# Optimization experiments

Measured on AMD Instinct MI355X. Metric: run time of the kernel, lower is better.

## Reference

```python
import jax, jax.numpy as jnp
import numpy as np
from jax import lax

B, R, C, K = 4, 512, 80, 100          # images, rois/img, fg classes, post_nms_top_k
NMS_TH, SCORE_TH = 0.3, 0.1
MEAN = jnp.zeros(4, jnp.float32)       # delta_mean
STD = jnp.ones(4, jnp.float32)         # delta_std
NEG = jnp.float32(-1e9)
DWH_CLIP = jnp.float32(4.135166556742356)  # log(1000/16), standard bbox_xform clip


def setup_inputs() -> dict:
    key = jax.random.key(0)
    k1, k2, k3, k4 = jax.random.split(key, 4)
    x1y1 = jax.random.uniform(k1, (B, R, 2), minval=0.0, maxval=800.0)
    wh = jax.random.uniform(k2, (B, R, 2), minval=16.0, maxval=220.0)
    batch_rois = jnp.concatenate([x1y1, jnp.minimum(x1y1 + wh, 1023.0)], axis=-1)
    bbox_score = jax.random.uniform(k3, (B * R, C + 1, 1, 1), dtype=jnp.float32)
    bbox_deltas = jax.random.normal(k4, (B * R, (C + 1) * 4, 1, 1), dtype=jnp.float32) * 0.2
    im_hw = jnp.full((B, 1, 1, 2), 1024, dtype=jnp.int32)
    return {"batch_rois": batch_rois, "bbox_score": bbox_score,
            "bbox_deltas": bbox_deltas, "im_hw": im_hw}


def _pairwise_iou(b):
    # b: [R, 4] (x1,y1,x2,y2) -> [R, R]
    area = (b[:, 2] - b[:, 0]) * (b[:, 3] - b[:, 1])
    lt = jnp.maximum(b[:, None, :2], b[None, :, :2])
    rb = jnp.minimum(b[:, None, 2:], b[None, :, 2:])
    wh = jnp.maximum(rb - lt, 0.0)
    inter = wh[..., 0] * wh[..., 1]
    return inter / (area[:, None] + area[None, :] - inter + 1e-9)


def _nms_one_class(boxes, scores):
    # boxes: [R,4], scores: [R] -> keep mask + score-sorted boxes/scores
    order = jnp.argsort(-scores)
    b = boxes[order]
    s = scores[order]
    iou = _pairwise_iou(b)  # [R, R]

    def body(sup, i):
        keep_i = jnp.logical_and(jnp.logical_not(sup[i]), s[i] > SCORE_TH)
        new = jnp.where(keep_i, jnp.logical_or(sup, iou[i] > NMS_TH), sup)
        new = new.at[i].set(sup[i])  # never self-suppress
        return new, keep_i

    _, keep = lax.scan(body, jnp.zeros(b.shape[0], bool), jnp.arange(b.shape[0]))
    return keep, b, s


def _decode(rois, deltas, hw):
    # rois: [R,4], deltas: [R,C,4], hw: [2] (h, w) -> decoded boxes [R,C,4]
    d = deltas * STD + MEAN
    w = rois[:, 2] - rois[:, 0]
    h = rois[:, 3] - rois[:, 1]
    cx = rois[:, 0] + 0.5 * w
    cy = rois[:, 1] + 0.5 * h
    dx, dy = d[..., 0], d[..., 1]
    dw = jnp.minimum(d[..., 2], DWH_CLIP)
    dh = jnp.minimum(d[..., 3], DWH_CLIP)
    pcx = dx * w[:, None] + cx[:, None]
    pcy = dy * h[:, None] + cy[:, None]
    pw = w[:, None] * jnp.exp(dw)
    ph = h[:, None] * jnp.exp(dh)
    x1 = jnp.clip(pcx - 0.5 * pw, 0.0, hw[1] - 1.0)
    y1 = jnp.clip(pcy - 0.5 * ph, 0.0, hw[0] - 1.0)
    x2 = jnp.clip(pcx + 0.5 * pw, 0.0, hw[1] - 1.0)
    y2 = jnp.clip(pcy + 0.5 * ph, 0.0, hw[0] - 1.0)
    return jnp.stack([x1, y1, x2, y2], axis=-1)


def reference(batch_rois, bbox_score, bbox_deltas, im_hw):
    scores = bbox_score.reshape(B, R, C + 1)[..., 1:]               # [B,R,C] (skip bg)
    deltas = bbox_deltas.reshape(B, R, C + 1, 4)[:, :, 1:, :]       # [B,R,C,4]
    hw = im_hw.reshape(B, 2).astype(jnp.float32)

    def per_image(rois, sc, dl, hw_i):
        boxes = _decode(rois, dl, hw_i)                              # [R,C,4]
        keep, bs, ss = jax.vmap(_nms_one_class)(
            jnp.swapaxes(boxes, 0, 1), sc.T)                         # [C,R]...
        cls = jnp.broadcast_to(jnp.arange(C, dtype=jnp.float32)[:, None], (C, R))
        flat_s = jnp.where(keep, ss, NEG).reshape(-1)                # [C*R]
        top_s, idx = lax.top_k(flat_s, K)
        tb = bs.reshape(-1, 4)[idx]
        tc = cls.reshape(-1)[idx]
        valid = top_s > NEG * 0.5
        row = jnp.concatenate([tb, top_s[:, None], tc[:, None]], axis=-1)  # [K,6]
        pad = jnp.concatenate([jnp.zeros((K, 5), jnp.float32),
                               -jnp.ones((K, 1), jnp.float32)], axis=-1)
        return jnp.where(valid[:, None], row, pad)

    return jax.vmap(per_image)(batch_rois, scores, deltas, hw)      # [B,K,6]
```

## Files before the change

kernel.cpp:

```cpp
#include <hip/hip_runtime.h>
#include <cstdint>

#define BB 4
#define RR 512
#define CC 80
#define KK 100
#define NMS_TH 0.3f
#define SCORE_TH 0.1f
#define DWH_CLIP 4.135166556742356f

typedef unsigned short u16;
typedef unsigned int u32;
typedef unsigned long long u64;

__device__ __forceinline__ u32 f32_sortable(float f) {
  u32 u = __float_as_uint(f);
  u32 mask = (u32)((int)u >> 31) | 0x80000000u;
  return u ^ mask;
}
__device__ __forceinline__ float sortable_to_f32(u32 s) {
  u32 u = (s & 0x80000000u) ? (s ^ 0x80000000u) : ~s;
  return __uint_as_float(u);
}

__global__ __launch_bounds__(512) void nms_fused(
    const float* __restrict__ rois,
    const float* __restrict__ scores,
    const float* __restrict__ deltas,
    const int*   __restrict__ im_hw,
    u64*   __restrict__ cand_key,
    float4* __restrict__ cand_box)
{
#pragma clang fp contract(off)
  const int bc = blockIdx.x;
  const int b = bc / CC, c = bc % CC;
  const int tid = threadIdx.x;
  const int lane = tid & 63, wv = tid >> 6;

  __shared__ u64    keyarr[RR];
  __shared__ float4 box_s[RR];
  __shared__ float  sco_s[RR];
  __shared__ u64    rmk[64];
  __shared__ u64    supacc;
  __shared__ float4 kbox[KK];
  __shared__ float  ksc[KK];
  __shared__ float  karea[KK];
  __shared__ int    nkept_s;

  const float fh = (float)im_hw[b * 2 + 0] - 1.0f;
  const float fw = (float)im_hw[b * 2 + 1] - 1.0f;

  {
    const float sc = scores[(b * RR + tid) * (CC + 1) + (c + 1)];
    u64 v = ((u64)(~f32_sortable(sc)) << 32) | (u32)tid;
    const u32 t = (u32)tid;
    for (u32 kk = 2; kk <= RR; kk <<= 1) {
      for (u32 j = kk >> 1; j > 0; j >>= 1) {
        u64 p;
        if (j >= 64) {
          keyarr[t] = v;
          __syncthreads();
          p = keyarr[t ^ j];
          __syncthreads();
        } else {
          p = __shfl_xor(v, (int)j);
        }
        bool up = ((t & kk) == 0);
        bool lower = ((t & j) == 0);
        bool takemin = (up == lower);
        bool pless = (p < v);
        v = (takemin == pless) ? p : v;
      }
    }
    keyarr[t] = v;
  }
  __syncthreads();

  {
    const u64 kv = keyarr[tid];
    const int r = (int)(kv & 0xFFFFFFFFull);
    const float sc = sortable_to_f32(~(u32)(kv >> 32));
    const float4 roi = *(const float4*)&rois[(b * RR + r) * 4];
    const int base = (b * RR + r) * (CC + 1) + (c + 1);
    const float4 d = *(const float4*)&deltas[base * 4];

    float w  = roi.z - roi.x;
    float h  = roi.w - roi.y;
    float cx = roi.x + 0.5f * w;
    float cy = roi.y + 0.5f * h;
    float dw = fminf(d.z, DWH_CLIP);
    float dh = fminf(d.w, DWH_CLIP);
    float pcx = d.x * w + cx;
    float pcy = d.y * h + cy;
    float pw = w * expf(dw);
    float ph = h * expf(dh);
    float hx = 0.5f * pw, hy = 0.5f * ph;
    float x1 = fminf(fmaxf(pcx - hx, 0.0f), fw);
    float y1 = fminf(fmaxf(pcy - hy, 0.0f), fh);
    float x2 = fminf(fmaxf(pcx + hx, 0.0f), fw);
    float y2 = fminf(fmaxf(pcy + hy, 0.0f), fh);

    box_s[tid] = make_float4(x1, y1, x2, y2);
    sco_s[tid] = sc;
    if (tid == 0) nkept_s = 0;
  }
  __syncthreads();

  int nk = 0;
  for (int w = 0; w < 8; ++w) {
    const float4 bx = box_s[w * 64 + lane];
    const float  sc = sco_s[w * 64 + lane];
    const float  ar = (bx.z - bx.x) * (bx.w - bx.y);
    const float  areps = ar + 1e-9f;

    if (tid < 64) rmk[tid] = 0ull;
    if (tid == 64) supacc = 0ull;
    __syncthreads();

    {
      u64 myrow = 0;
      #pragma unroll
      for (int jj = 0; jj < 8; ++jj) {
        const int j = wv * 8 + jj;
        const float4 cb = box_s[w * 64 + j];
        const float ca = (cb.z - cb.x) * (cb.w - cb.y);
        float iw = fminf(bx.z, cb.z) - fmaxf(bx.x, cb.x);
        float ih = fminf(bx.w, cb.w) - fmaxf(bx.y, cb.y);
        iw = fmaxf(iw, 0.0f);
        ih = fmaxf(ih, 0.0f);
        const float inter = iw * ih;
        const float S = ca + areps;
        bool yes = inter * 4.3333247f > S;
        const bool no = inter * 4.3333420f < S;
        if (__any(!(yes || no))) {
          const float denom = ((ca + ar) - inter) + 1e-9f;
          const bool pe = inter / denom > NMS_TH;
          yes = (yes || no) ? yes : pe;
        }
        myrow |= yes ? (1ull << j) : 0ull;
      }
      myrow &= ~((2ull << lane) - 1ull);
      if (myrow) atomicOr(&rmk[lane], myrow);
    }

    {
      bool sup = false;
      for (int k = wv; k < nk; k += 8) {
        const float4 kb = kbox[k];
        const float  ka = karea[k];
        float iw = fminf(bx.z, kb.z) - fmaxf(bx.x, kb.x);
        float ih = fminf(bx.w, kb.w) - fmaxf(bx.y, kb.y);
        iw = fmaxf(iw, 0.0f);
        ih = fmaxf(ih, 0.0f);
        const float inter = iw * ih;
        const float S = ka + areps;
        bool yes = inter * 4.3333247f > S;
        const bool no = inter * 4.3333420f < S;
        if (__any(!(yes || no))) {
          const float denom = ((ka + ar) - inter) + 1e-9f;
          const bool pe = inter / denom > NMS_TH;
          yes = (yes || no) ? yes : pe;
        }
        sup = sup || yes;
      }
      const u64 bal = __ballot(sup);
      if (lane == 0 && bal) atomicOr(&supacc, bal);
    }
    __syncthreads();

    if (wv == 0) {
      u64 todo = __ballot(sc > SCORE_TH) & ~supacc;
      int nkl = nk;
      while (todo) {
        const int i = __ffsll((long long)todo) - 1;
        if (lane == 0) {
          const float4 kb = box_s[w * 64 + i];
          kbox[nkl] = kb;
          ksc[nkl] = sco_s[w * 64 + i];
          karea[nkl] = (kb.z - kb.x) * (kb.w - kb.y);
        }
        ++nkl;
        if (nkl >= KK) break;
        const u64 ri = rmk[i];
        todo &= ~((2ull << i) - 1ull);
        todo &= ~ri;
      }
      if (lane == 0) nkept_s = nkl;
    }
    __syncthreads();
    nk = nkept_s;
    if (nk >= KK) break;
  }

  if (tid < KK) {
    const int k = tid;
    u64 kv; float4 obx;
    if (k < nk) {
      kv = ((u64)(~f32_sortable(ksc[k])) << 32) | ((u64)(u32)c << 16) | (u32)k;
      obx = kbox[k];
    } else {
      kv = ((u64)(~f32_sortable(-1e9f)) << 32) | ((u64)(u32)c << 16) | (u32)k;
      obx = make_float4(0.f, 0.f, 0.f, 0.f);
    }
    cand_key[bc * KK + k] = kv;
    cand_box[bc * KK + k] = obx;
  }
}

__device__ __forceinline__ void sort128(u64* smallkeys, int tid) {
  u64 v = (tid < 128) ? smallkeys[tid] : ~0ull;
  const u32 t = (u32)tid;
  for (u32 kk = 2; kk <= 128; kk <<= 1) {
    for (u32 j = kk >> 1; j > 0; j >>= 1) {
      if (j >= 64) {
        if (tid < 128) smallkeys[t] = v;
        __syncthreads();
        u64 p = (tid < 128) ? smallkeys[t ^ j] : ~0ull;
        __syncthreads();
        if (tid < 128) {
          bool up = ((t & kk) == 0);
          bool lower = ((t & j) == 0);
          bool takemin = (up == lower);
          bool pless = (p < v);
          v = (takemin == pless) ? p : v;
        }
      } else if (tid < 128) {
        u64 p = __shfl_xor(v, (int)j);
        bool up = ((t & kk) == 0);
        bool lower = ((t & j) == 0);
        bool takemin = (up == lower);
        bool pless = (p < v);
        v = (takemin == pless) ? p : v;
      }
    }
  }
  if (tid < 128) smallkeys[t] = v;
  __syncthreads();
}

__global__ __launch_bounds__(1024) void topk_select(
    const u64* __restrict__ cand_key,
    const float4* __restrict__ cand_box,
    float* __restrict__ out)
{
  const int b = blockIdx.x;
  const int tid = threadIdx.x;
  const int lane = tid & 63, wv = tid >> 6;
  const int N = CC * KK;
  const u64* __restrict__ keys_g = cand_key + (size_t)b * N;

  __shared__ u16 candA[CC * KK];
  __shared__ u16 candB[CC * KK];
  __shared__ u32 whist[16][256];
  __shared__ u32 bins[256];
  __shared__ u64 smallkeys[128];
  __shared__ int ncand_s, rank_s, q_s;
  __shared__ u32 cnt_s;

  if (tid == 0) { ncand_s = N; rank_s = KK - 1; }

  u16* cur = candA;
  u16* oth = candB;
  bool first = true;
  int d = 7;
  for (;;) {
    for (int t = tid; t < 16 * 256; t += 1024) ((u32*)whist)[t] = 0;
    __syncthreads();
    const int nc = first ? N : ncand_s;
    const int sh = d * 8;
    for (int t0 = 0; t0 < nc; t0 += 1024) {
      const int t = t0 + tid;
      if (t < nc) {
        const int idx = first ? t : (int)cur[t];
        u32 dig = (u32)((keys_g[idx] >> sh) & 0xFF);
        atomicAdd(&whist[wv][dig], 1u);
      }
    }
    __syncthreads();
    if (tid < 256) {
      u32 s = 0;
      #pragma unroll
      for (int w = 0; w < 16; ++w) s += whist[w][tid];
      bins[tid] = s;
    }
    __syncthreads();
    if (wv == 0) {
      u32 c0 = bins[lane * 4 + 0], c1 = bins[lane * 4 + 1];
      u32 c2 = bins[lane * 4 + 2], c3 = bins[lane * 4 + 3];
      u32 lsum = c0 + c1 + c2 + c3;
      u32 incl = lsum;
      #pragma unroll
      for (int off = 1; off < 64; off <<= 1) {
        u32 v = __shfl_up(incl, off);
        if (lane >= off) incl += v;
      }
      u32 excl = incl - lsum;
      int rk = rank_s;
      u32 s0 = excl, s1 = excl + c0, s2 = s1 + c1, s3 = s2 + c2;
      int q = -1; u32 nr = 0;
      if (rk >= (int)s0 && rk < (int)(s0 + c0)) { q = lane * 4 + 0; nr = rk - s0; }
      else if (rk >= (int)s1 && rk < (int)(s1 + c1)) { q = lane * 4 + 1; nr = rk - s1; }
      else if (rk >= (int)s2 && rk < (int)(s2 + c2)) { q = lane * 4 + 2; nr = rk - s2; }
      else if (rk >= (int)s3 && rk < (int)(s3 + c3)) { q = lane * 4 + 3; nr = rk - s3; }
      if (q >= 0) { q_s = q; rank_s = (int)nr; }
    }
    if (tid == 0) cnt_s = 0;
    __syncthreads();
    const int q = q_s;
    for (int t0 = 0; t0 < nc; t0 += 1024) {
      const int t = t0 + tid;
      int idx = 0; bool m = false;
      if (t < nc) {
        idx = first ? t : (int)cur[t];
        m = ((int)((keys_g[idx] >> sh) & 0xFF) == q);
      }
      u64 bal = __ballot(m);
      u32 base = 0;
      if (lane == 0 && bal) base = atomicAdd(&cnt_s, (u32)__popcll(bal));
      base = __shfl(base, 0);
      if (m) oth[base + (u32)__popcll(bal & ((1ull << lane) - 1ull))] = (u16)idx;
    }
    __syncthreads();
    if (tid == 0) ncand_s = (int)cnt_s;
    { u16* tmp = cur; cur = oth; oth = tmp; }
    first = false;
    __syncthreads();
    if (ncand_s <= 128 || d == 0) break;
    --d;
  }

  u64 T;
  const int nc2 = ncand_s;
  if (nc2 == 1) {
    T = keys_g[cur[0]];
  } else {
    if (tid < 128) smallkeys[tid] = (tid < nc2) ? keys_g[cur[tid]] : ~0ull;
    __syncthreads();
    sort128(smallkeys, tid);
    T = smallkeys[rank_s];
    __syncthreads();
  }

  if (tid == 0) cnt_s = 0;
  if (tid < 128) smallkeys[tid] = ~0ull;
  __syncthreads();
  for (int t0 = 0; t0 < N; t0 += 1024) {
    const int t = t0 + tid;
    u64 k = 0; bool m = false;
    if (t < N) { k = keys_g[t]; m = (k <= T); }
    u64 bal = __ballot(m);
    u32 base = 0;
    if (lane == 0 && bal) base = atomicAdd(&cnt_s, (u32)__popcll(bal));
    base = __shfl(base, 0);
    if (m) {
      u32 p = base + (u32)__popcll(bal & ((1ull << lane) - 1ull));
      if (p < 128) smallkeys[p] = k;
    }
  }
  __syncthreads();

  sort128(smallkeys, tid);

  if (tid < KK) {
    const u64 kv = smallkeys[tid];
    const float s = sortable_to_f32(~(u32)(kv >> 32));
    float x1 = 0.f, y1 = 0.f, x2 = 0.f, y2 = 0.f, so = 0.f, cf = -1.0f;
    if (s > -5.0e8f) {
      int c = (int)((kv >> 16) & 0xFFFFull);
      int k = (int)(kv & 0xFFFFull);
      float4 bx = cand_box[((size_t)b * CC + c) * KK + k];
      x1 = bx.x; y1 = bx.y; x2 = bx.z; y2 = bx.w;
      so = s; cf = (float)c;
    }
    float* o = out + ((size_t)b * KK + tid) * 6;
    o[0] = x1; o[1] = y1; o[2] = x2; o[3] = y2; o[4] = so; o[5] = cf;
  }
}

extern "C" void kernel_launch(void* const* d_in, const int* in_sizes, int n_in,
                              void* d_out, int out_size, void* d_ws, size_t ws_size,
                              hipStream_t stream) {
  (void)in_sizes; (void)n_in; (void)out_size; (void)ws_size;
  const float* rois   = (const float*)d_in[0];
  const float* scores = (const float*)d_in[1];
  const float* deltas = (const float*)d_in[2];
  const int*   im_hw  = (const int*)d_in[3];

  char* ws = (char*)d_ws;
  u64*    cand_key = (u64*)ws;
  float4* cand_box = (float4*)(ws + 256000);

  nms_fused<<<BB * CC, 512, 0, stream>>>(rois, scores, deltas, im_hw,
                                         cand_key, cand_box);
  topk_select<<<BB, 1024, 0, stream>>>(cand_key, cand_box, (float*)d_out);
}
```

Baseline: 63.28 us.

## Fuse NMS and top-k into one kernel with last-block-done reduction

Merges the per-class NMS kernel and the per-image top-k selection kernel into a single launch. A global atomic counter per image lets the last finishing block run the radix-select top-k. The 512-element bitonic sort now keeps 8 keys per thread in registers, so fewer shared-memory round trips and barriers are needed. The intra-window suppression masks are precomputed for all 8 windows up front, and the greedy loop reads them with readlane instead of from shared memory. Top-k now runs with 512 threads instead of 1024 and needs a memset launch and threadfences, which may offset the saved kernel launch.

```diff
diff --git a/kernel.cpp b/kernel.cpp
--- a/kernel.cpp
+++ b/kernel.cpp
@@ -21,190 +21,6 @@
 __device__ __forceinline__ float sortable_to_f32(u32 s) {
   u32 u = (s & 0x80000000u) ? (s ^ 0x80000000u) : ~s;
   return __uint_as_float(u);
-}
-
-__global__ __launch_bounds__(512) void nms_fused(
-    const float* __restrict__ rois,
-    const float* __restrict__ scores,
-    const float* __restrict__ deltas,
-    const int*   __restrict__ im_hw,
-    u64*   __restrict__ cand_key,
-    float4* __restrict__ cand_box)
-{
-#pragma clang fp contract(off)
-  const int bc = blockIdx.x;
-  const int b = bc / CC, c = bc % CC;
-  const int tid = threadIdx.x;
-  const int lane = tid & 63, wv = tid >> 6;
-
-  __shared__ u64    keyarr[RR];
-  __shared__ float4 box_s[RR];
-  __shared__ float  sco_s[RR];
-  __shared__ u64    rmk[64];
-  __shared__ u64    supacc;
-  __shared__ float4 kbox[KK];
-  __shared__ float  ksc[KK];
-  __shared__ float  karea[KK];
-  __shared__ int    nkept_s;
-
-  const float fh = (float)im_hw[b * 2 + 0] - 1.0f;
-  const float fw = (float)im_hw[b * 2 + 1] - 1.0f;
-
-  {
-    const float sc = scores[(b * RR + tid) * (CC + 1) + (c + 1)];
-    u64 v = ((u64)(~f32_sortable(sc)) << 32) | (u32)tid;
-    const u32 t = (u32)tid;
-    for (u32 kk = 2; kk <= RR; kk <<= 1) {
-      for (u32 j = kk >> 1; j > 0; j >>= 1) {
-        u64 p;
-        if (j >= 64) {
-          keyarr[t] = v;
-          __syncthreads();
-          p = keyarr[t ^ j];
-          __syncthreads();
-        } else {
-          p = __shfl_xor(v, (int)j);
-        }
-        bool up = ((t & kk) == 0);
-        bool lower = ((t & j) == 0);
-        bool takemin = (up == lower);
-        bool pless = (p < v);
-        v = (takemin == pless) ? p : v;
-      }
-    }
-    keyarr[t] = v;
-  }
-  __syncthreads();
-
-  {
-    const u64 kv = keyarr[tid];
-    const int r = (int)(kv & 0xFFFFFFFFull);
-    const float sc = sortable_to_f32(~(u32)(kv >> 32));
-    const float4 roi = *(const float4*)&rois[(b * RR + r) * 4];
-    const int base = (b * RR + r) * (CC + 1) + (c + 1);
-    const float4 d = *(const float4*)&deltas[base * 4];
-
-    float w  = roi.z - roi.x;
-    float h  = roi.w - roi.y;
-    float cx = roi.x + 0.5f * w;
-    float cy = roi.y + 0.5f * h;
-    float dw = fminf(d.z, DWH_CLIP);
-    float dh = fminf(d.w, DWH_CLIP);
-    float pcx = d.x * w + cx;
-    float pcy = d.y * h + cy;
-    float pw = w * expf(dw);
-    float ph = h * expf(dh);
-    float hx = 0.5f * pw, hy = 0.5f * ph;
-    float x1 = fminf(fmaxf(pcx - hx, 0.0f), fw);
-    float y1 = fminf(fmaxf(pcy - hy, 0.0f), fh);
-    float x2 = fminf(fmaxf(pcx + hx, 0.0f), fw);
-    float y2 = fminf(fmaxf(pcy + hy, 0.0f), fh);
-
-    box_s[tid] = make_float4(x1, y1, x2, y2);
-    sco_s[tid] = sc;
-    if (tid == 0) nkept_s = 0;
-  }
-  __syncthreads();
-
-  int nk = 0;
-  for (int w = 0; w < 8; ++w) {
-    const float4 bx = box_s[w * 64 + lane];
-    const float  sc = sco_s[w * 64 + lane];
-    const float  ar = (bx.z - bx.x) * (bx.w - bx.y);
-    const float  areps = ar + 1e-9f;
-
-    if (tid < 64) rmk[tid] = 0ull;
-    if (tid == 64) supacc = 0ull;
-    __syncthreads();
-
-    {
-      u64 myrow = 0;
-      #pragma unroll
-      for (int jj = 0; jj < 8; ++jj) {
-        const int j = wv * 8 + jj;
-        const float4 cb = box_s[w * 64 + j];
-        const float ca = (cb.z - cb.x) * (cb.w - cb.y);
-        float iw = fminf(bx.z, cb.z) - fmaxf(bx.x, cb.x);
-        float ih = fminf(bx.w, cb.w) - fmaxf(bx.y, cb.y);
-        iw = fmaxf(iw, 0.0f);
-        ih = fmaxf(ih, 0.0f);
-        const float inter = iw * ih;
-        const float S = ca + areps;
-        bool yes = inter * 4.3333247f > S;
-        const bool no = inter * 4.3333420f < S;
-        if (__any(!(yes || no))) {
-          const float denom = ((ca + ar) - inter) + 1e-9f;
-          const bool pe = inter / denom > NMS_TH;
-          yes = (yes || no) ? yes : pe;
-        }
-        myrow |= yes ? (1ull << j) : 0ull;
-      }
-      myrow &= ~((2ull << lane) - 1ull);
-      if (myrow) atomicOr(&rmk[lane], myrow);
-    }
-
-    {
-      bool sup = false;
-      for (int k = wv; k < nk; k += 8) {
-        const float4 kb = kbox[k];
-        const float  ka = karea[k];
-        float iw = fminf(bx.z, kb.z) - fmaxf(bx.x, kb.x);
-        float ih = fminf(bx.w, kb.w) - fmaxf(bx.y, kb.y);
-        iw = fmaxf(iw, 0.0f);
-        ih = fmaxf(ih, 0.0f);
-        const float inter = iw * ih;
-        const float S = ka + areps;
-        bool yes = inter * 4.3333247f > S;
-        const bool no = inter * 4.3333420f < S;
-        if (__any(!(yes || no))) {
-          const float denom = ((ka + ar) - inter) + 1e-9f;
-          const bool pe = inter / denom > NMS_TH;
-          yes = (yes || no) ? yes : pe;
-        }
-        sup = sup || yes;
-      }
-      const u64 bal = __ballot(sup);
-      if (lane == 0 && bal) atomicOr(&supacc, bal);
-    }
-    __syncthreads();
-
-    if (wv == 0) {
-      u64 todo = __ballot(sc > SCORE_TH) & ~supacc;
-      int nkl = nk;
-      while (todo) {
-        const int i = __ffsll((long long)todo) - 1;
-        if (lane == 0) {
-          const float4 kb = box_s[w * 64 + i];
-          kbox[nkl] = kb;
-          ksc[nkl] = sco_s[w * 64 + i];
-          karea[nkl] = (kb.z - kb.x) * (kb.w - kb.y);
-        }
-        ++nkl;
-        if (nkl >= KK) break;
-        const u64 ri = rmk[i];
-        todo &= ~((2ull << i) - 1ull);
-        todo &= ~ri;
-      }
-      if (lane == 0) nkept_s = nkl;
-    }
-    __syncthreads();
-    nk = nkept_s;
-    if (nk >= KK) break;
-  }
-
-  if (tid < KK) {
-    const int k = tid;
-    u64 kv; float4 obx;
-    if (k < nk) {
-      kv = ((u64)(~f32_sortable(ksc[k])) << 32) | ((u64)(u32)c << 16) | (u32)k;
-      obx = kbox[k];
-    } else {
-      kv = ((u64)(~f32_sortable(-1e9f)) << 32) | ((u64)(u32)c << 16) | (u32)k;
-      obx = make_float4(0.f, 0.f, 0.f, 0.f);
-    }
-    cand_key[bc * KK + k] = kv;
-    cand_box[bc * KK + k] = obx;
-  }
 }
 
 __device__ __forceinline__ void sort128(u64* smallkeys, int tid) {
@@ -238,22 +54,226 @@
   __syncthreads();
 }
 
-__global__ __launch_bounds__(1024) void topk_select(
-    const u64* __restrict__ cand_key,
-    const float4* __restrict__ cand_box,
+__global__ __launch_bounds__(512) void nms_topk(
+    const float* __restrict__ rois,
+    const float* __restrict__ scores,
+    const float* __restrict__ deltas,
+    const int*   __restrict__ im_hw,
+    u32*   __restrict__ done_cnt,
+    u64*   __restrict__ cand_key,
+    float4* __restrict__ cand_box,
     float* __restrict__ out)
 {
-  const int b = blockIdx.x;
+#pragma clang fp contract(off)
+  const int bc = blockIdx.x;
+  const int b = bc / CC, c = bc % CC;
   const int tid = threadIdx.x;
   const int lane = tid & 63, wv = tid >> 6;
+
+  __shared__ __align__(16) char pool[42240];
+  float4* box_s = (float4*)pool;
+  float*  sco_s = (float*)(pool + 8192);
+  u64*    rmk_w = (u64*)(pool + 10240);
+  float4* kbox  = (float4*)(pool + 14336);
+  float*  ksc   = (float*)(pool + 15936);
+  float*  karea = (float*)(pool + 16336);
+  __shared__ u64 supacc_arr[8];
+  __shared__ int nkept_s, lastflag;
+
+  const float fh = (float)im_hw[b * 2 + 0] - 1.0f;
+  const float fw = (float)im_hw[b * 2 + 1] - 1.0f;
+
+  sco_s[tid] = scores[(b * RR + tid) * (CC + 1) + (c + 1)];
+  __syncthreads();
+
+  u64 k[8];
+  #pragma unroll
+  for (int r = 0; r < 8; ++r) {
+    const int e = r * 64 + lane;
+    k[r] = ((u64)(~f32_sortable(sco_s[e])) << 32) | (u32)e;
+  }
+  #pragma unroll
+  for (u32 kk2 = 2; kk2 <= 512; kk2 <<= 1) {
+    #pragma unroll
+    for (u32 j = 256; j > 0; j >>= 1) {
+      if (j > (kk2 >> 1)) continue;
+      if (j >= 64) {
+        const int dj = (int)(j >> 6);
+        #pragma unroll
+        for (int r = 0; r < 8; ++r) {
+          if ((r & dj) == 0) {
+            const int r2 = r | dj;
+            const bool up = (((u32)(r * 64) & kk2) == 0);
+            u64 a = k[r], b2 = k[r2];
+            const bool sw = up ? (a > b2) : (a < b2);
+            if (sw) { k[r] = b2; k[r2] = a; }
+          }
+        }
+      } else {
+        #pragma unroll
+        for (int r = 0; r < 8; ++r) {
+          u64 p = __shfl_xor(k[r], (int)j);
+          const u32 e = (u32)(r * 64) + (u32)lane;
+          const bool up = ((e & kk2) == 0);
+          const bool lower = (((u32)lane & j) == 0);
+          const bool takemin = (up == lower);
+          const bool pless = (p < k[r]);
+          k[r] = (takemin == pless) ? p : k[r];
+        }
+      }
+    }
+  }
+  __syncthreads();
+
+  {
+    u64 kv = k[0];
+    #pragma unroll
+    for (int r = 1; r < 8; ++r) if (wv == r) kv = k[r];
+    const int rr = (int)(kv & 0xFFFFFFFFull);
+    const float sc = sortable_to_f32(~(u32)(kv >> 32));
+    const float4 roi = *(const float4*)&rois[(b * RR + rr) * 4];
+    const int base = (b * RR + rr) * (CC + 1) + (c + 1);
+    const float4 d = *(const float4*)&deltas[base * 4];
+
+    float w  = roi.z - roi.x;
+    float h  = roi.w - roi.y;
+    float cx = roi.x + 0.5f * w;
+    float cy = roi.y + 0.5f * h;
+    float dw = fminf(d.z, DWH_CLIP);
+    float dh = fminf(d.w, DWH_CLIP);
+    float pcx = d.x * w + cx;
+    float pcy = d.y * h + cy;
+    float pw = w * expf(dw);
+    float ph = h * expf(dh);
+    float hx = 0.5f * pw, hy = 0.5f * ph;
+    float x1 = fminf(fmaxf(pcx - hx, 0.0f), fw);
+    float y1 = fminf(fmaxf(pcy - hy, 0.0f), fh);
+    float x2 = fminf(fmaxf(pcx + hx, 0.0f), fw);
+    float y2 = fminf(fmaxf(pcy + hy, 0.0f), fh);
+
+    box_s[tid] = make_float4(x1, y1, x2, y2);
+    sco_s[tid] = sc;
+    if (tid == 0) nkept_s = 0;
+  }
+  __syncthreads();
+
+  {
+    const float4 bxr = box_s[wv * 64 + lane];
+    const float ar = (bxr.z - bxr.x) * (bxr.w - bxr.y);
+    const float areps = ar + 1e-9f;
+    u64 myrow = 0;
+    for (int j = 0; j < 64; ++j) {
+      const float4 cb = box_s[wv * 64 + j];
+      const float ca = (cb.z - cb.x) * (cb.w - cb.y);
+      float iw = fminf(bxr.z, cb.z) - fmaxf(bxr.x, cb.x);
+      float ih = fminf(bxr.w, cb.w) - fmaxf(bxr.y, cb.y);
+      iw = fmaxf(iw, 0.0f);
+      ih = fmaxf(ih, 0.0f);
+      const float inter = iw * ih;
+      const float S = ca + areps;
+      bool yes = inter * 4.3333247f > S;
+      const bool no = inter * 4.3333420f < S;
+      if (__any(!(yes || no))) {
+        const float denom = ((ca + ar) - inter) + 1e-9f;
+        const bool pe = inter / denom > NMS_TH;
+        yes = (yes || no) ? yes : pe;
+      }
+      myrow |= yes ? (1ull << j) : 0ull;
+    }
+    myrow &= ~((2ull << lane) - 1ull);
+    rmk_w[wv * 64 + lane] = myrow;
+  }
+  __syncthreads();
+
+  int nk = 0;
+  for (int w = 0; w < 8 && nk < KK; ++w) {
+    {
+      const float4 bxc = box_s[w * 64 + lane];
+      const float ar = (bxc.z - bxc.x) * (bxc.w - bxc.y);
+      const float areps = ar + 1e-9f;
+      bool sup = false;
+      for (int kx = wv; kx < nk; kx += 8) {
+        const float4 kb = kbox[kx];
+        const float ka = karea[kx];
+        float iw = fminf(bxc.z, kb.z) - fmaxf(bxc.x, kb.x);
+        float ih = fminf(bxc.w, kb.w) - fmaxf(bxc.y, kb.y);
+        iw = fmaxf(iw, 0.0f);
+        ih = fmaxf(ih, 0.0f);
+        const float inter = iw * ih;
+        const float S = ka + areps;
+        bool yes = inter * 4.3333247f > S;
+        const bool no = inter * 4.3333420f < S;
+        if (__any(!(yes || no))) {
+          const float denom = ((ka + ar) - inter) + 1e-9f;
+          const bool pe = inter / denom > NMS_TH;
+          yes = (yes || no) ? yes : pe;
+        }
+        sup = sup || yes;
+      }
+      const u64 bal = __ballot(sup);
+      if (lane == 0) supacc_arr[wv] = bal;
+    }
+    __syncthreads();
+
+    if (wv == 0) {
+      u64 sup = supacc_arr[0];
+      #pragma unroll
+      for (int ww = 1; ww < 8; ++ww) sup |= supacc_arr[ww];
+      const u64 rm = rmk_w[w * 64 + lane];
+      const u32 rlo = (u32)rm, rhi = (u32)(rm >> 32);
+      u64 todo = __ballot(sco_s[w * 64 + lane] > SCORE_TH) & ~sup;
+      int nkl = nk;
+      while (todo) {
+        const int i = __ffsll((long long)todo) - 1;
+        if (lane == 0) {
+          const float4 kb = box_s[w * 64 + i];
+          kbox[nkl] = kb;
+          ksc[nkl] = sco_s[w * 64 + i];
+          karea[nkl] = (kb.z - kb.x) * (kb.w - kb.y);
+        }
+        ++nkl;
+        if (nkl >= KK) break;
+        const u32 rl = (u32)__builtin_amdgcn_readlane((int)rlo, i);
+        const u32 rh = (u32)__builtin_amdgcn_readlane((int)rhi, i);
+        todo &= ~((2ull << i) - 1ull);
+        todo &= ~(((u64)rh << 32) | rl);
+      }
+      if (lane == 0) nkept_s = nkl;
+    }
+    __syncthreads();
+    nk = nkept_s;
+  }
+
+  if (tid < KK) {
+    const int kx = tid;
+    u64 kv; float4 obx;
+    if (kx < nk) {
+      kv = ((u64)(~f32_sortable(ksc[kx])) << 32) | ((u64)(u32)c << 16) | (u32)kx;
+      obx = kbox[kx];
+    } else {
+      kv = ((u64)(~f32_sortable(-1e9f)) << 32) | ((u64)(u32)c << 16) | (u32)kx;
+      obx = make_float4(0.f, 0.f, 0.f, 0.f);
+    }
+    cand_key[bc * KK + kx] = kv;
+    cand_box[bc * KK + kx] = obx;
+  }
+
+  __threadfence();
+  if (tid == 0) {
+    const u32 old = atomicAdd(&done_cnt[b], 1u);
+    lastflag = (old == CC - 1) ? 1 : 0;
+  }
+  __syncthreads();
+  if (!lastflag) return;
+  __threadfence();
+
   const int N = CC * KK;
   const u64* __restrict__ keys_g = cand_key + (size_t)b * N;
-
-  __shared__ u16 candA[CC * KK];
-  __shared__ u16 candB[CC * KK];
-  __shared__ u32 whist[16][256];
-  __shared__ u32 bins[256];
-  __shared__ u64 smallkeys[128];
+  u16* candA = (u16*)pool;
+  u16* candB = (u16*)(pool + 16000);
+  u32* whist = (u32*)(pool + 32000);
+  u32* bins  = (u32*)(pool + 40192);
+  u64* smallkeys = (u64*)(pool + 41216);
   __shared__ int ncand_s, rank_s, q_s;
   __shared__ u32 cnt_s;
 
@@ -264,23 +284,23 @@
   bool first = true;
   int d = 7;
   for (;;) {
-    for (int t = tid; t < 16 * 256; t += 1024) ((u32*)whist)[t] = 0;
+    for (int t = tid; t < 8 * 256; t += 512) whist[t] = 0;
     __syncthreads();
     const int nc = first ? N : ncand_s;
     const int sh = d * 8;
-    for (int t0 = 0; t0 < nc; t0 += 1024) {
+    for (int t0 = 0; t0 < nc; t0 += 512) {
       const int t = t0 + tid;
       if (t < nc) {
         const int idx = first ? t : (int)cur[t];
         u32 dig = (u32)((keys_g[idx] >> sh) & 0xFF);
-        atomicAdd(&whist[wv][dig], 1u);
+        atomicAdd(&whist[wv * 256 + dig], 1u);
       }
     }
     __syncthreads();
     if (tid < 256) {
       u32 s = 0;
       #pragma unroll
-      for (int w = 0; w < 16; ++w) s += whist[w][tid];
+      for (int ww = 0; ww < 8; ++ww) s += whist[ww * 256 + tid];
       bins[tid] = s;
     }
     __syncthreads();
@@ -307,7 +327,7 @@
     if (tid == 0) cnt_s = 0;
     __syncthreads();
     const int q = q_s;
-    for (int t0 = 0; t0 < nc; t0 += 1024) {
+    for (int t0 = 0; t0 < nc; t0 += 512) {
       const int t = t0 + tid;
       int idx = 0; bool m = false;
       if (t < nc) {
@@ -344,17 +364,17 @@
   if (tid == 0) cnt_s = 0;
   if (tid < 128) smallkeys[tid] = ~0ull;
   __syncthreads();
-  for (int t0 = 0; t0 < N; t0 += 1024) {
+  for (int t0 = 0; t0 < N; t0 += 512) {
     const int t = t0 + tid;
-    u64 k = 0; bool m = false;
-    if (t < N) { k = keys_g[t]; m = (k <= T); }
+    u64 kk = 0; bool m = false;
+    if (t < N) { kk = keys_g[t]; m = (kk <= T); }
     u64 bal = __ballot(m);
     u32 base = 0;
     if (lane == 0 && bal) base = atomicAdd(&cnt_s, (u32)__popcll(bal));
     base = __shfl(base, 0);
     if (m) {
       u32 p = base + (u32)__popcll(bal & ((1ull << lane) - 1ull));
-      if (p < 128) smallkeys[p] = k;
+      if (p < 128) smallkeys[p] = kk;
     }
   }
   __syncthreads();
@@ -366,11 +386,11 @@
     const float s = sortable_to_f32(~(u32)(kv >> 32));
     float x1 = 0.f, y1 = 0.f, x2 = 0.f, y2 = 0.f, so = 0.f, cf = -1.0f;
     if (s > -5.0e8f) {
-      int c = (int)((kv >> 16) & 0xFFFFull);
-      int k = (int)(kv & 0xFFFFull);
-      float4 bx = cand_box[((size_t)b * CC + c) * KK + k];
+      int cc2 = (int)((kv >> 16) & 0xFFFFull);
+      int kx = (int)(kv & 0xFFFFull);
+      float4 bx = cand_box[((size_t)b * CC + cc2) * KK + kx];
       x1 = bx.x; y1 = bx.y; x2 = bx.z; y2 = bx.w;
-      so = s; cf = (float)c;
+      so = s; cf = (float)cc2;
     }
     float* o = out + ((size_t)b * KK + tid) * 6;
     o[0] = x1; o[1] = y1; o[2] = x2; o[3] = y2; o[4] = so; o[5] = cf;
@@ -387,10 +407,12 @@
   const int*   im_hw  = (const int*)d_in[3];
 
   char* ws = (char*)d_ws;
-  u64*    cand_key = (u64*)ws;
-  float4* cand_box = (float4*)(ws + 256000);
-
-  nms_fused<<<BB * CC, 512, 0, stream>>>(rois, scores, deltas, im_hw,
-                                         cand_key, cand_box);
-  topk_select<<<BB, 1024, 0, stream>>>(cand_key, cand_box, (float*)d_out);
+  u32*    done_cnt = (u32*)ws;
+  u64*    cand_key = (u64*)(ws + 4096);
+  float4* cand_box = (float4*)(ws + 4096 + 256000);
+
+  hipMemsetAsync(done_cnt, 0, BB * sizeof(u32), stream);
+  nms_topk<<<BB * CC, 512, 0, stream>>>(rois, scores, deltas, im_hw,
+                                        done_cnt, cand_key, cand_box,
+                                        (float*)d_out);
 }
```

Result: slower. 138.4 us (+118.7%).
